# Performance work log

Hardware: AMD Instinct MI355X
Metric: run time of the kernel (lower is better)

## Reference

```python
import jax, jax.numpy as jnp
import numpy as np

B, DIM, H, W = 4, 64, 256, 256
HEADS = 8
HID = int(DIM * 2.66)  # 170, IEL hidden_features
EPS_LN = 1e-6


def setup_inputs() -> dict:
    key = jax.random.key(0)
    ks = jax.random.split(key, 16)
    r = lambda k, shape, s=0.02: jax.random.normal(k, shape, jnp.float32) * s
    return {
        "x": jax.random.normal(ks[0], (B, DIM, H, W), jnp.float32),
        "y": jax.random.normal(ks[1], (B, DIM, H, W), jnp.float32),
        # shared channels-first LayerNorm params
        "ln_w": jnp.ones((DIM,), jnp.float32),
        "ln_b": jnp.zeros((DIM,), jnp.float32),
        # CAB params (bias=False)
        "temperature": jnp.ones((HEADS, 1, 1), jnp.float32),
        "wq": r(ks[2], (DIM, DIM)),           # 1x1 conv: [out, in]
        "wq_dw": r(ks[3], (DIM, 1, 3, 3)),    # depthwise 3x3
        "wkv": r(ks[4], (2 * DIM, DIM)),
        "wkv_dw": r(ks[5], (2 * DIM, 1, 3, 3)),
        "w_proj": r(ks[6], (DIM, DIM)),
        # IEL params (bias=False)
        "w_in": r(ks[7], (2 * HID, DIM)),
        "w_dw": r(ks[8], (2 * HID, 1, 3, 3)),
        "w_dw1": r(ks[9], (HID, 1, 3, 3)),
        "w_dw2": r(ks[10], (HID, 1, 3, 3)),
        "w_out": r(ks[11], (DIM, HID)),
    }


def conv1x1(x, w):
    # x: [b,c,h,w], w: [o,c]
    return jnp.einsum('oc,bchw->bohw', w, x)


def dwconv3(x, w):
    # depthwise 3x3, SAME padding; w: [C,1,3,3]
    return jax.lax.conv_general_dilated(
        x, w, window_strides=(1, 1), padding='SAME',
        feature_group_count=x.shape[1],
        dimension_numbers=('NCHW', 'OIHW', 'NCHW'))


def layernorm_cf(x, w, b):
    # channels-first LayerNorm: mean/biased-var over channel dim
    u = jnp.mean(x, axis=1, keepdims=True)
    s = jnp.mean((x - u) ** 2, axis=1, keepdims=True)
    xn = (x - u) / jnp.sqrt(s + EPS_LN)
    return w[None, :, None, None] * xn + b[None, :, None, None]


def l2norm(x):
    # torch F.normalize(dim=-1): x / max(||x||, 1e-12)
    n = jnp.sqrt(jnp.sum(x * x, axis=-1, keepdims=True))
    return x / jnp.maximum(n, 1e-12)


def cab(x, y, temperature, wq, wq_dw, wkv, wkv_dw, w_proj):
    b, c, h, w = x.shape
    q = dwconv3(conv1x1(x, wq), wq_dw)
    kv = dwconv3(conv1x1(y, wkv), wkv_dw)
    k, v = kv[:, :c], kv[:, c:]
    ch = c // HEADS  # channels per head
    q = l2norm(q.reshape(b, HEADS, ch, h * w))
    k = l2norm(k.reshape(b, HEADS, ch, h * w))
    v = v.reshape(b, HEADS, ch, h * w)
    attn = jnp.einsum('bhce,bhde->bhcd', q, k) * temperature[None]  # [b,H,ch,ch]
    attn = jax.nn.softmax(attn, axis=-1)
    out = jnp.einsum('bhcd,bhde->bhce', attn, v).reshape(b, c, h, w)
    return conv1x1(out, w_proj)


def iel(x, w_in, w_dw, w_dw1, w_dw2, w_out):
    x = conv1x1(x, w_in)
    d = dwconv3(x, w_dw)
    x1, x2 = d[:, :HID], d[:, HID:]
    x1 = jnp.tanh(dwconv3(x1, w_dw1)) + x1
    x2 = jnp.tanh(dwconv3(x2, w_dw2)) + x2
    return conv1x1(x1 * x2, w_out)


def reference(x, y, ln_w, ln_b, temperature, wq, wq_dw, wkv, wkv_dw, w_proj,
              w_in, w_dw, w_dw1, w_dw2, w_out):
    # I_LCA block forward
    x = x + cab(layernorm_cf(x, ln_w, ln_b), layernorm_cf(y, ln_w, ln_b),
                temperature, wq, wq_dw, wkv, wkv_dw, w_proj)
    x = x + iel(layernorm_cf(x, ln_w, ln_b), w_in, w_dw, w_dw1, w_dw2, w_out)
    return x
```

## Files before the change

kernel.cpp:

```cpp
#include <hip/hip_runtime.h>
#include <hip/hip_bf16.h>

typedef __hip_bfloat16 bf16;
typedef unsigned short u16;
typedef unsigned int u32;
typedef __attribute__((ext_vector_type(8))) unsigned short ushort8;
typedef __attribute__((ext_vector_type(4))) unsigned int uint4_t;
typedef __attribute__((ext_vector_type(8))) short bf16x8;
typedef __attribute__((ext_vector_type(4))) short bf16x4;
typedef __attribute__((ext_vector_type(4))) float f32x4;
typedef __attribute__((ext_vector_type(2))) _Float16 half2_t;

#define PL 65536
#define EPS_LN 1e-6f

#if __has_builtin(__builtin_amdgcn_fdot2)
#define USE_FDOT2 1
#else
#define USE_FDOT2 0
#endif

__device__ __forceinline__ float fast_tanh(float v){
  float e = __expf(2.f*v);
  return 1.f - 2.f/(e+1.f);
}
__device__ __forceinline__ u16 f2bf(float f){
  bf16 h = __float2bfloat16(f);
  return __builtin_bit_cast(u16, h);
}
__device__ __forceinline__ float bf2f(u16 v){
  u32 u = ((u32)v) << 16;
  return __builtin_bit_cast(float, u);
}
__device__ __forceinline__ u16 f2h(float f){
  _Float16 h = (_Float16)f;
  return __builtin_bit_cast(u16, h);
}
__device__ __forceinline__ float h2f(u16 v){
  _Float16 h = __builtin_bit_cast(_Float16, v);
  return (float)h;
}
__device__ __forceinline__ float dot2h(u32 wpair, u32 kpair, float acc){
#if USE_FDOT2
  return __builtin_amdgcn_fdot2(__builtin_bit_cast(half2_t, wpair),
                                __builtin_bit_cast(half2_t, kpair), acc, false);
#else
  float a0 = h2f((u16)(wpair & 0xffff)), a1 = h2f((u16)(wpair >> 16));
  float k0 = h2f((u16)(kpair & 0xffff)), k1 = h2f((u16)(kpair >> 16));
  return acc + a0*k0 + a1*k1;
#endif
}
__device__ __forceinline__ u32 alignhalf(u32 hi, u32 lo){
  return (lo >> 16) | (hi << 16);
}

__global__ void convert_w(const float* __restrict__ wq, const float* __restrict__ wkv,
                          const float* __restrict__ win, const float* __restrict__ wout,
                          const float* __restrict__ wproj,
                          u16* __restrict__ Wq, u16* __restrict__ Wkv,
                          u16* __restrict__ Wp0, u16* __restrict__ Wp1,
                          u16* __restrict__ Wproj, u16* __restrict__ Wh){
  int stride = gridDim.x * 256;
  int gid = blockIdx.x * 256 + threadIdx.x;
  for (int i = gid; i < 64*64;  i += stride) Wq[i]  = f2bf(wq[i]);
  for (int i = gid; i < 128*64; i += stride) Wkv[i] = f2bf(wkv[i]);
  for (int i = gid; i < 176*64; i += stride) {
    int r = i >> 6, c = i & 63;
    Wp0[i] = (r < 85) ? f2bf(win[r*64+c]) : ((r < 170) ? f2bf(win[(85+r)*64+c]) : 0);
    Wp1[i] = (r < 85) ? f2bf(win[(85+r)*64+c]) : ((r < 170) ? f2bf(win[(170+r)*64+c]) : 0);
  }
  for (int i = gid; i < 64*64; i += stride) Wproj[i] = f2bf(wproj[i]);
  for (int i = gid; i < 64*192; i += stride) {
    int o = i / 192, c = i % 192;
    Wh[i] = (c < 170) ? f2bf(wout[o*170 + c]) : 0;
  }
}

__global__ __launch_bounds__(256) void ln_gemm(
    const float* __restrict__ x, const float* __restrict__ lnw,
    const float* __restrict__ lnb, const u16* __restrict__ W,
    u16* __restrict__ out, int MT, int Mvalid, int fmt) {
  int b  = blockIdx.y;
  int p0 = blockIdx.x * 256;
  int tid = threadIdx.x;
  int lane = tid & 63, wv = tid >> 6;
  __shared__ u16 shX[256][72];
  {
    const float* xb = x + ((size_t)b * 64) * PL + p0 + tid;
    float xn[64];
    float mu = 0.f;
    #pragma unroll
    for (int c = 0; c < 64; ++c) { xn[c] = xb[(size_t)c * PL]; mu += xn[c]; }
    mu *= (1.f/64.f);
    float var = 0.f;
    #pragma unroll
    for (int c = 0; c < 64; ++c) { float d = xn[c]-mu; var += d*d; }
    var *= (1.f/64.f);
    float inv = rsqrtf(var + EPS_LN);
    #pragma unroll
    for (int c8 = 0; c8 < 8; ++c8) {
      ushort8 pk;
      #pragma unroll
      for (int j = 0; j < 8; ++j)
        pk[j] = f2bf((xn[c8*8+j]-mu)*inv*lnw[c8*8+j] + lnb[c8*8+j]);
      *reinterpret_cast<ushort8*>(&shX[tid][c8*8]) = pk;
    }
  }
  __syncthreads();
  int col = lane & 15, kg = lane >> 4;
  int n0 = wv * 64;
  bf16x8 bfr[4][2];
  #pragma unroll
  for (int nt = 0; nt < 4; ++nt)
    #pragma unroll
    for (int kh = 0; kh < 2; ++kh)
      bfr[nt][kh] = *reinterpret_cast<const bf16x8*>(&shX[n0 + nt*16 + col][kh*32 + kg*8]);
  for (int mt = 0; mt < MT; ++mt) {
    bf16x8 a0 = *reinterpret_cast<const bf16x8*>(&W[(mt*16+col)*64      + kg*8]);
    bf16x8 a1 = *reinterpret_cast<const bf16x8*>(&W[(mt*16+col)*64 + 32 + kg*8]);
    #pragma unroll
    for (int nt = 0; nt < 4; ++nt) {
      f32x4 acc = {0.f,0.f,0.f,0.f};
      acc = __builtin_amdgcn_mfma_f32_16x16x32_bf16(a0, bfr[nt][0], acc, 0,0,0);
      acc = __builtin_amdgcn_mfma_f32_16x16x32_bf16(a1, bfr[nt][1], acc, 0,0,0);
      int mbase = mt*16 + kg*4;
      #pragma unroll
      for (int r = 0; r < 4; ++r) {
        int ch = mbase + r;
        if (ch < Mvalid)
          out[((size_t)b*Mvalid + ch)*PL + p0 + n0 + nt*16 + col] =
              fmt ? f2h(acc[r]) : f2bf(acc[r]);
      }
    }
  }
}

__global__ __launch_bounds__(256) void dwconv3v(
    const u16* __restrict__ in, const float* __restrict__ w9,
    u16* __restrict__ out, int C) {
  int plane = blockIdx.y;
  int cch = plane % C;
  int y0 = blockIdx.x * 8;
  int tid = threadIdx.x;
  const u16* ip = in + (size_t)plane * PL;
  __shared__ u16 sh[10][272];
  #pragma unroll
  for (int i = 0; i < 2; ++i) {
    int idx = tid + i*256;
    if (idx < 320) {
      int r = idx >> 5, seg = idx & 31;
      int gy = y0 - 1 + r;
      ushort8 v = {0,0,0,0,0,0,0,0};
      if (gy >= 0 && gy < 256)
        v = *reinterpret_cast<const ushort8*>(ip + gy*256 + seg*8);
      *reinterpret_cast<ushort8*>(&sh[r][8 + seg*8]) = v;
    }
  }
  if (tid < 10) { sh[tid][7] = 0; sh[tid][264] = 0; }
  __syncthreads();
  float wk[9];
  #pragma unroll
  for (int i=0;i<9;++i) wk[i] = w9[cch*9+i];
  int lr = tid >> 5, xs = (tid & 31) * 8;
  float row[3][10];
  #pragma unroll
  for (int i = 0; i < 3; ++i) {
    ushort8 m = *reinterpret_cast<const ushort8*>(&sh[lr+i][8+xs]);
    row[i][0] = bf2f(sh[lr+i][7+xs]);
    #pragma unroll
    for (int j=0;j<8;++j) row[i][1+j] = bf2f((u16)m[j]);
    row[i][9] = bf2f(sh[lr+i][16+xs]);
  }
  ushort8 o;
  #pragma unroll
  for (int j = 0; j < 8; ++j) {
    float a = 0.f;
    #pragma unroll
    for (int i=0;i<3;++i)
      #pragma unroll
      for (int k=0;k<3;++k) a += wk[i*3+k]*row[i][j+k];
    o[j] = f2bf(a);
  }
  int gy = y0 + lr;
  *reinterpret_cast<ushort8*>(out + (size_t)plane*PL + gy*256 + xs) = o;
}

__global__ __launch_bounds__(256) void attn_reduce1(
    const bf16* __restrict__ q, const bf16* __restrict__ kv,
    float* __restrict__ part) {
  int bh = blockIdx.y;
  int b = bh >> 3, h = bh & 7;
  int s = blockIdx.x;
  int t = threadIdx.x;
  int p = s*2048 + t*8;
  const u16* qb = reinterpret_cast<const u16*>(q)  + ((size_t)b*64  + h*8) * PL + p;
  const u16* kb = reinterpret_cast<const u16*>(kv) + ((size_t)b*128 + h*8) * PL + p;
  ushort8 vq[8], vk[8];
  #pragma unroll
  for (int c=0;c<8;++c) {
    vq[c] = *reinterpret_cast<const ushort8*>(qb + (size_t)c*PL);
    vk[c] = *reinterpret_cast<const ushort8*>(kb + (size_t)c*PL);
  }
  float acc[80];
  #pragma unroll
  for (int i=0;i<80;++i) acc[i]=0.f;
  #pragma unroll
  for (int e = 0; e < 8; ++e) {
    float qe[8], ke[8];
    #pragma unroll
    for (int c=0;c<8;++c) { qe[c]=bf2f((u16)vq[c][e]); ke[c]=bf2f((u16)vk[c][e]); }
    #pragma unroll
    for (int c=0;c<8;++c)
      #pragma unroll
      for (int d=0;d<8;++d) acc[c*8+d] += qe[c]*ke[d];
    #pragma unroll
    for (int c=0;c<8;++c) { acc[64+c] += qe[c]*qe[c]; acc[72+c] += ke[c]*ke[c]; }
  }
  __shared__ float lds[4][80];
  int lane = t & 63, wv = t >> 6;
  #pragma unroll
  for (int i=0;i<80;++i) {
    float v = acc[i];
    for (int off=32; off; off>>=1) v += __shfl_down(v, off);
    if (lane==0) lds[wv][i]=v;
  }
  __syncthreads();
  if (t < 80)
    part[((size_t)bh*32 + s)*80 + t] = lds[0][t]+lds[1][t]+lds[2][t]+lds[3][t];
}

__global__ void attn_reduce2(const float* __restrict__ part, float* __restrict__ red) {
  int bh = blockIdx.x; int t = threadIdx.x;
  if (t < 80) {
    float v = 0.f;
    for (int s=0;s<32;++s) v += part[((size_t)bh*32+s)*80+t];
    red[bh*80+t]=v;
  }
}

__global__ void attn_softmax(const float* __restrict__ red, const float* __restrict__ temp,
                             float* __restrict__ attn) {
  int bh = threadIdx.x;
  if (bh >= 32) return;
  int h = bh & 7;
  const float* r = red + bh*80;
  float nq[8], nk[8];
  for (int c=0;c<8;++c) nq[c] = fmaxf(sqrtf(r[64+c]), 1e-12f);
  for (int d=0;d<8;++d) nk[d] = fmaxf(sqrtf(r[72+d]), 1e-12f);
  float tm = temp[h];
  for (int c=0;c<8;++c) {
    float a[8]; float m=-1e30f;
    for (int d=0;d<8;++d){ a[d] = r[c*8+d]/(nq[c]*nk[d]) * tm; m=fmaxf(m,a[d]); }
    float ss=0.f;
    for (int d=0;d<8;++d){ a[d]=__expf(a[d]-m); ss+=a[d]; }
    float inv=1.f/ss;
    for (int d=0;d<8;++d) attn[bh*64 + c*8 + d] = a[d]*inv;
  }
}

__global__ __launch_bounds__(256) void attn_pv_proj(
    const bf16* __restrict__ kv, const float* __restrict__ attnb,
    const u16* __restrict__ Wp, const float* __restrict__ x,
    float* __restrict__ out) {
  int b  = blockIdx.y;
  int p0 = blockIdx.x * 256;
  int tid = threadIdx.x;
  int lane = tid & 63, wv = tid >> 6;
  __shared__ float at[512];
  __shared__ u16 shX[256][72];
  for (int i=tid; i<512; i+=256) at[i]=attnb[b*512+i];
  __syncthreads();
  {
    int pix = p0 + tid;
    const bf16* vb = kv + ((size_t)b*128 + 64)*PL + pix;
    #pragma unroll
    for (int h=0;h<8;++h){
      float vv[8];
      #pragma unroll
      for (int d=0;d<8;++d) vv[d]=__bfloat162float(vb[(size_t)(h*8+d)*PL]);
      ushort8 pk;
      #pragma unroll
      for (int c=0;c<8;++c){
        float acc=0.f;
        #pragma unroll
        for (int d=0;d<8;++d) acc += at[h*64+c*8+d]*vv[d];
        pk[c] = f2bf(acc);
      }
      *reinterpret_cast<ushort8*>(&shX[tid][h*8]) = pk;
    }
  }
  __syncthreads();
  int col = lane & 15, kg = lane >> 4;
  int n0 = wv * 64;
  bf16x8 bfr[4][2];
  #pragma unroll
  for (int nt = 0; nt < 4; ++nt)
    #pragma unroll
    for (int kh = 0; kh < 2; ++kh)
      bfr[nt][kh] = *reinterpret_cast<const bf16x8*>(&shX[n0 + nt*16 + col][kh*32 + kg*8]);
  #pragma unroll
  for (int mt = 0; mt < 4; ++mt) {
    bf16x8 a0 = *reinterpret_cast<const bf16x8*>(&Wp[(mt*16+col)*64      + kg*8]);
    bf16x8 a1 = *reinterpret_cast<const bf16x8*>(&Wp[(mt*16+col)*64 + 32 + kg*8]);
    #pragma unroll
    for (int nt = 0; nt < 4; ++nt) {
      f32x4 acc = {0.f,0.f,0.f,0.f};
      acc = __builtin_amdgcn_mfma_f32_16x16x32_bf16(a0, bfr[nt][0], acc, 0,0,0);
      acc = __builtin_amdgcn_mfma_f32_16x16x32_bf16(a1, bfr[nt][1], acc, 0,0,0);
      #pragma unroll
      for (int r = 0; r < 4; ++r) {
        int o = mt*16 + kg*4 + r;
        size_t idx = ((size_t)(b*64 + o))*PL + p0 + n0 + nt*16 + col;
        out[idx] = x[idx] + acc[r];
      }
    }
  }
}

__global__ __launch_bounds__(256) void iel_gate2(
    const u16* __restrict__ t, const float* __restrict__ wdw,
    const float* __restrict__ wdw1, const float* __restrict__ wdw2,
    u16* __restrict__ P, int hcbase) {
  int pj = blockIdx.y;
  int b = pj / 85, j = pj % 85;
  int hc = hcbase + j;
  int bx = blockIdx.x;
  int y0 = (bx >> 2) * 32;
  int x0 = (bx & 3) * 64;
  int tid = threadIdx.x;

  __shared__ u16 sT[2][36][80];
  __shared__ u16 sD[2][34][72];

  const u16* t1 = t + (size_t)(b*170 + j) * PL;
  const u16* t2 = t + (size_t)(b*170 + 85 + j) * PL;

  #pragma unroll
  for (int it = 0; it < 3; ++it) {
    int idx = tid + it*256;
    if (idx < 720) {
      int pl = idx / 360, rem = idx % 360;
      int r = rem / 10, ch = rem % 10;
      int gy = y0 + r - 2;
      int gxb = x0 - 8 + ch*8;
      ushort8 v = {0,0,0,0,0,0,0,0};
      if (gy >= 0 && gy < 256 && gxb >= 0 && gxb <= 248)
        v = *reinterpret_cast<const ushort8*>((pl ? t2 : t1) + gy*256 + gxb);
      *reinterpret_cast<ushort8*>(&sT[pl][r][ch*8]) = v;
    }
  }
  __syncthreads();

  #pragma unroll
  for (int it = 0; it < 3; ++it) {
    int idx = tid + it*256;
    if (idx < 612) {
      int pl = idx / 306, rem = idx % 306;
      int r = rem / 9, si = rem % 9;
      int gy = y0 + r - 1;
      const float* kp = wdw + (pl ? (170+hc) : hc)*9;
      u32 k01[3], k2z[3];
      #pragma unroll
      for (int i=0;i<3;++i){
        k01[i] = (u32)f2h(kp[i*3+0]) | ((u32)f2h(kp[i*3+1]) << 16);
        k2z[i] = (u32)f2h(kp[i*3+2]);
      }
      float a[8];
      #pragma unroll
      for (int jj=0;jj<8;++jj) a[jj]=0.f;
      #pragma unroll
      for (int i = 0; i < 3; ++i) {
        ushort8 A0 = *reinterpret_cast<const ushort8*>(&sT[pl][r+i][si*8]);
        ushort8 A1 = *reinterpret_cast<const ushort8*>(&sT[pl][r+i][si*8+8]);
        uint4_t wa = __builtin_bit_cast(uint4_t, A0);
        uint4_t wb = __builtin_bit_cast(uint4_t, A1);
        u32 R1=wa.y, R2=wa.z, R3=wa.w, R4=wb.x, R5=wb.y, R6=wb.z;
        u32 prs[10] = { alignhalf(R2,R1), R2, alignhalf(R3,R2), R3,
                        alignhalf(R4,R3), R4, alignhalf(R5,R4), R5,
                        alignhalf(R6,R5), R6 };
        #pragma unroll
        for (int jj = 0; jj < 8; ++jj)
          a[jj] = dot2h(prs[jj+2], k2z[i], dot2h(prs[jj], k01[i], a[jj]));
      }
      int gx0 = x0 + si*8 - 4;
      bool rowok = (gy >= 0 && gy < 256);
      ushort8 dv;
      #pragma unroll
      for (int jj = 0; jj < 8; ++jj) {
        int gx = gx0 + jj;
        bool ok = rowok && gx >= 0 && gx < 256;
        dv[jj] = ok ? f2h(a[jj]) : (u16)0;
      }
      *reinterpret_cast<ushort8*>(&sD[pl][r][si*8]) = dv;
    }
  }
  __syncthreads();

  int ry = tid >> 3, seg = tid & 7;
  float x1[8], x2[8];
  #pragma unroll
  for (int pl = 0; pl < 2; ++pl) {
    const float* kp = (pl ? wdw2 : wdw1) + hc*9;
    u32 k01[3], k2z[3];
    #pragma unroll
    for (int i=0;i<3;++i){
      k01[i] = (u32)f2h(kp[i*3+0]) | ((u32)f2h(kp[i*3+1]) << 16);
      k2z[i] = (u32)f2h(kp[i*3+2]);
    }
    float a[8];
    #pragma unroll
    for (int jj=0;jj<8;++jj) a[jj]=0.f;
    float dc[8];
    #pragma unroll
    for (int i = 0; i < 3; ++i) {
      ushort8 A0 = *reinterpret_cast<const ushort8*>(&sD[pl][ry+i][seg*8]);
      ushort8 A1 = *reinterpret_cast<const ushort8*>(&sD[pl][ry+i][seg*8+8]);
      uint4_t wa = __builtin_bit_cast(uint4_t, A0);
      uint4_t wb = __builtin_bit_cast(uint4_t, A1);
      u32 R1=wa.y, R2=wa.z, R3=wa.w, R4=wb.x, R5=wb.y, R6=wb.z;
      u32 prs[10] = { alignhalf(R2,R1), R2, alignhalf(R3,R2), R3,
                      alignhalf(R4,R3), R4, alignhalf(R5,R4), R5,
                      alignhalf(R6,R5), R6 };
      #pragma unroll
      for (int jj = 0; jj < 8; ++jj)
        a[jj] = dot2h(prs[jj+2], k2z[i], dot2h(prs[jj], k01[i], a[jj]));
      if (i == 1) {
        u32 cw[4] = { wa.z, wa.w, wb.x, wb.y };
        #pragma unroll
        for (int jj = 0; jj < 8; ++jj) {
          u32 wrd = cw[(jj+4)/2 - 2];
          u16 hv = (jj & 1) ? (u16)(wrd >> 16) : (u16)(wrd & 0xffff);
          dc[jj] = h2f(hv);
        }
      }
    }
    #pragma unroll
    for (int jj = 0; jj < 8; ++jj) {
      float g = fast_tanh(a[jj]) + dc[jj];
      if (pl) x2[jj] = g; else x1[jj] = g;
    }
  }
  ushort8 o;
  #pragma unroll
  for (int jj = 0; jj < 8; ++jj) o[jj] = f2bf(x1[jj]*x2[jj]);
  int gy = y0 + ry;
  *reinterpret_cast<ushort8*>(
      P + ((size_t)(b*170 + hcbase + j))*PL + gy*256 + x0 + seg*8) = o;
}

__global__ __launch_bounds__(256) void iel_gemm(
    const u16* __restrict__ Wh, const u16* __restrict__ P,
    float* __restrict__ out) {
  int b  = blockIdx.y;
  int p0 = blockIdx.x * 256;
  int tid = threadIdx.x;
  int lane = tid & 63, wv = tid >> 6;
  int col = lane & 15, kg = lane >> 4;
  int n0 = wv * 64;
  __shared__ u16 shP[256][36];
  f32x4 acc[4][4];
  #pragma unroll
  for (int mt=0;mt<4;++mt)
    #pragma unroll
    for (int nt=0;nt<4;++nt) acc[mt][nt] = (f32x4){0.f,0.f,0.f,0.f};

  int kk = tid & 31, q = tid >> 5;
  for (int c = 0; c < 6; ++c) {
    int hcl = c*32 + kk;
    ushort8 v[4];
    if (hcl < 170) {
      const u16* src = P + (size_t)(b*170 + hcl)*PL + p0 + q*32;
      #pragma unroll
      for (int jj=0;jj<4;++jj) v[jj] = *reinterpret_cast<const ushort8*>(src + jj*8);
    } else {
      #pragma unroll
      for (int jj=0;jj<4;++jj) v[jj] = (ushort8){0,0,0,0,0,0,0,0};
    }
    __syncthreads();
    #pragma unroll
    for (int jj=0;jj<4;++jj)
      #pragma unroll
      for (int i=0;i<8;++i) shP[q*32 + jj*8 + i][kk] = v[jj][i];
    __syncthreads();
    #pragma unroll
    for (int nt = 0; nt < 4; ++nt) {
      int px = n0 + nt*16 + col;
      const bf16x4* pp = reinterpret_cast<const bf16x4*>(&shP[px][kg*8]);
      bf16x4 plo = pp[0], phi = pp[1];
      bf16x8 bfrag;
      #pragma unroll
      for (int jj=0;jj<4;++jj){ bfrag[jj]=plo[jj]; bfrag[4+jj]=phi[jj]; }
      #pragma unroll
      for (int mt = 0; mt < 4; ++mt) {
        bf16x8 a = *reinterpret_cast<const bf16x8*>(&Wh[(mt*16+col)*192 + c*32 + kg*8]);
        acc[mt][nt] = __builtin_amdgcn_mfma_f32_16x16x32_bf16(a, bfrag, acc[mt][nt], 0,0,0);
      }
    }
  }
  #pragma unroll
  for (int mt=0; mt<4; ++mt)
    #pragma unroll
    for (int nt=0; nt<4; ++nt)
      #pragma unroll
      for (int r=0; r<4; ++r){
        int o = mt*16 + kg*4 + r;
        size_t idx = ((size_t)(b*64 + o))*PL + p0 + n0 + nt*16 + col;
        out[idx] += acc[mt][nt][r];
      }
}

extern "C" void kernel_launch(void* const* d_in, const int* in_sizes, int n_in,
                              void* d_out, int out_size, void* d_ws, size_t ws_size,
                              hipStream_t stream) {
  const float* x      = (const float*)d_in[0];
  const float* y      = (const float*)d_in[1];
  const float* lnw    = (const float*)d_in[2];
  const float* lnb    = (const float*)d_in[3];
  const float* temp   = (const float*)d_in[4];
  const float* wq     = (const float*)d_in[5];
  const float* wq_dw  = (const float*)d_in[6];
  const float* wkv    = (const float*)d_in[7];
  const float* wkv_dw = (const float*)d_in[8];
  const float* wproj  = (const float*)d_in[9];
  const float* w_in   = (const float*)d_in[10];
  const float* w_dw   = (const float*)d_in[11];
  const float* w_dw1  = (const float*)d_in[12];
  const float* w_dw2  = (const float*)d_in[13];
  const float* w_out  = (const float*)d_in[14];

  char* base = (char*)d_ws;
  u16* Wq_b    = (u16*)(base + 0);
  u16* Wkv_b   = (u16*)(base + 8192);
  u16* Wp0     = (u16*)(base + 24576);
  u16* Wp1     = (u16*)(base + 47104);
  u16* Wproj_b = (u16*)(base + 69632);
  u16* Wh      = (u16*)(base + 77824);
  char* A = base + 131072;

  u16*  kvpre = (u16*)A;
  u16*  kvd   = (u16*)(A + 89128960);
  u16*  qpre  = (u16*)A;
  u16*  qd    = (u16*)(A + 33554432);
  float* part = (float*)A;
  float* red  = (float*)(A + 1048576);
  float* attnb= (float*)(A + 1572864);
  u16*  tbuf  = (u16*)A;
  u16*  Pbuf  = (u16*)(A + 89128960);
  float* xmid = (float*)d_out;

  convert_w<<<64, 256, 0, stream>>>(wq, wkv, w_in, w_out, wproj,
                                    Wq_b, Wkv_b, Wp0, Wp1, Wproj_b, Wh);

  ln_gemm<<<dim3(256,4), 256, 0, stream>>>(y, lnw, lnb, Wkv_b, kvpre, 8, 128, 0);
  dwconv3v<<<dim3(32,512), 256, 0, stream>>>(kvpre, wkv_dw, kvd, 128);
  ln_gemm<<<dim3(256,4), 256, 0, stream>>>(x, lnw, lnb, Wq_b, qpre, 4, 64, 0);
  dwconv3v<<<dim3(32,256), 256, 0, stream>>>(qpre, wq_dw, qd, 64);
  attn_reduce1<<<dim3(32,32), 256, 0, stream>>>((const bf16*)qd, (const bf16*)kvd, part);
  attn_reduce2<<<32, 128, 0, stream>>>(part, red);
  attn_softmax<<<1, 64, 0, stream>>>(red, temp, attnb);
  attn_pv_proj<<<dim3(256,4), 256, 0, stream>>>((const bf16*)kvd, attnb, Wproj_b, x, xmid);

  ln_gemm<<<dim3(256,4), 256, 0, stream>>>(xmid, lnw, lnb, Wp0, tbuf, 11, 170, 1);
  iel_gate2<<<dim3(32,340), 256, 0, stream>>>(tbuf, w_dw, w_dw1, w_dw2, Pbuf, 0);
  ln_gemm<<<dim3(256,4), 256, 0, stream>>>(xmid, lnw, lnb, Wp1, tbuf, 11, 170, 1);
  iel_gate2<<<dim3(32,340), 256, 0, stream>>>(tbuf, w_dw, w_dw1, w_dw2, Pbuf, 85);
  iel_gemm<<<dim3(256,4), 256, 0, stream>>>(Wh, Pbuf, xmid);
}
```

Measured before the change: 462.9 us.

## Fuse second LayerNorm into proj epilogue, merge softmax kernels, reorder plane layout

The attention projection epilogue now also computes the residual-stream LayerNorm and writes a pixel-major bf16 normalized tensor. A new gemm_pm kernel consumes that tensor for both IEL input GEMMs, so xmid is no longer re-read and re-normalized twice. The attention reduce and softmax kernels are merged into one launch. kv and P planes are stored channel-major across the batch, and iel_gate2 remaps block indices to change scheduling order. This adds an extra pixel-major write and changes access strides. The xnb buffer shares its offset with Pbuf and is read after Pbuf is partly written, which may be an aliasing hazard.

```diff
diff --git a/kernel.cpp b/kernel.cpp
--- a/kernel.cpp
+++ b/kernel.cpp
@@ -5,6 +5,7 @@
 typedef unsigned short u16;
 typedef unsigned int u32;
 typedef __attribute__((ext_vector_type(8))) unsigned short ushort8;
+typedef __attribute__((ext_vector_type(4))) unsigned short us4;
 typedef __attribute__((ext_vector_type(4))) unsigned int uint4_t;
 typedef __attribute__((ext_vector_type(8))) short bf16x8;
 typedef __attribute__((ext_vector_type(4))) short bf16x4;
@@ -79,7 +80,7 @@
 __global__ __launch_bounds__(256) void ln_gemm(
     const float* __restrict__ x, const float* __restrict__ lnw,
     const float* __restrict__ lnb, const u16* __restrict__ W,
-    u16* __restrict__ out, int MT, int Mvalid, int fmt) {
+    u16* __restrict__ out, int MT, int Mvalid) {
   int b  = blockIdx.y;
   int p0 = blockIdx.x * 256;
   int tid = threadIdx.x;
@@ -128,8 +129,48 @@
       for (int r = 0; r < 4; ++r) {
         int ch = mbase + r;
         if (ch < Mvalid)
-          out[((size_t)b*Mvalid + ch)*PL + p0 + n0 + nt*16 + col] =
-              fmt ? f2h(acc[r]) : f2bf(acc[r]);
+          out[((size_t)b*Mvalid + ch)*PL + p0 + n0 + nt*16 + col] = f2bf(acc[r]);
+      }
+    }
+  }
+}
+
+__global__ __launch_bounds__(256) void gemm_pm(
+    const u16* __restrict__ xn, const u16* __restrict__ W,
+    u16* __restrict__ out, int MT, int Mvalid) {
+  int b  = blockIdx.y;
+  int p0 = blockIdx.x * 256;
+  int tid = threadIdx.x;
+  int lane = tid & 63, wv = tid >> 6;
+  __shared__ u16 shX[256][72];
+  const u16* src = xn + ((size_t)b * PL + p0) * 64;
+  #pragma unroll
+  for (int c8 = 0; c8 < 8; ++c8)
+    *reinterpret_cast<ushort8*>(&shX[tid][c8*8]) =
+        *reinterpret_cast<const ushort8*>(src + (size_t)tid*64 + c8*8);
+  __syncthreads();
+  int col = lane & 15, kg = lane >> 4;
+  int n0 = wv * 64;
+  bf16x8 bfr[4][2];
+  #pragma unroll
+  for (int nt = 0; nt < 4; ++nt)
+    #pragma unroll
+    for (int kh = 0; kh < 2; ++kh)
+      bfr[nt][kh] = *reinterpret_cast<const bf16x8*>(&shX[n0 + nt*16 + col][kh*32 + kg*8]);
+  for (int mt = 0; mt < MT; ++mt) {
+    bf16x8 a0 = *reinterpret_cast<const bf16x8*>(&W[(mt*16+col)*64      + kg*8]);
+    bf16x8 a1 = *reinterpret_cast<const bf16x8*>(&W[(mt*16+col)*64 + 32 + kg*8]);
+    #pragma unroll
+    for (int nt = 0; nt < 4; ++nt) {
+      f32x4 acc = {0.f,0.f,0.f,0.f};
+      acc = __builtin_amdgcn_mfma_f32_16x16x32_bf16(a0, bfr[nt][0], acc, 0,0,0);
+      acc = __builtin_amdgcn_mfma_f32_16x16x32_bf16(a1, bfr[nt][1], acc, 0,0,0);
+      int mbase = mt*16 + kg*4;
+      #pragma unroll
+      for (int r = 0; r < 4; ++r) {
+        int ch = mbase + r;
+        if (ch < Mvalid)
+          out[((size_t)b*Mvalid + ch)*PL + p0 + n0 + nt*16 + col] = f2h(acc[r]);
       }
     }
   }
@@ -137,9 +178,10 @@
 
 __global__ __launch_bounds__(256) void dwconv3v(
     const u16* __restrict__ in, const float* __restrict__ w9,
-    u16* __restrict__ out, int C) {
+    u16* __restrict__ out, int C, int cb) {
   int plane = blockIdx.y;
   int cch = plane % C;
+  int bb  = plane / C;
   int y0 = blockIdx.x * 8;
   int tid = threadIdx.x;
   const u16* ip = in + (size_t)plane * PL;
@@ -182,24 +224,25 @@
     o[j] = f2bf(a);
   }
   int gy = y0 + lr;
-  *reinterpret_cast<ushort8*>(out + (size_t)plane*PL + gy*256 + xs) = o;
+  int oplane = cb ? (cch*4 + bb) : plane;
+  *reinterpret_cast<ushort8*>(out + (size_t)oplane*PL + gy*256 + xs) = o;
 }
 
 __global__ __launch_bounds__(256) void attn_reduce1(
-    const bf16* __restrict__ q, const bf16* __restrict__ kv,
+    const u16* __restrict__ q, const u16* __restrict__ kv,
     float* __restrict__ part) {
   int bh = blockIdx.y;
   int b = bh >> 3, h = bh & 7;
   int s = blockIdx.x;
   int t = threadIdx.x;
   int p = s*2048 + t*8;
-  const u16* qb = reinterpret_cast<const u16*>(q)  + ((size_t)b*64  + h*8) * PL + p;
-  const u16* kb = reinterpret_cast<const u16*>(kv) + ((size_t)b*128 + h*8) * PL + p;
+  const u16* qb = q  + ((size_t)b*64 + h*8) * PL + p;
+  const u16* kb = kv + ((size_t)(h*8)*4 + b) * PL + p;
   ushort8 vq[8], vk[8];
   #pragma unroll
   for (int c=0;c<8;++c) {
     vq[c] = *reinterpret_cast<const ushort8*>(qb + (size_t)c*PL);
-    vk[c] = *reinterpret_cast<const ushort8*>(kb + (size_t)c*PL);
+    vk[c] = *reinterpret_cast<const ushort8*>(kb + (size_t)c*4*PL);
   }
   float acc[80];
   #pragma unroll
@@ -229,55 +272,58 @@
     part[((size_t)bh*32 + s)*80 + t] = lds[0][t]+lds[1][t]+lds[2][t]+lds[3][t];
 }
 
-__global__ void attn_reduce2(const float* __restrict__ part, float* __restrict__ red) {
+__global__ void attn_finish(const float* __restrict__ part, const float* __restrict__ temp,
+                            float* __restrict__ attn) {
   int bh = blockIdx.x; int t = threadIdx.x;
+  __shared__ float red[80];
   if (t < 80) {
     float v = 0.f;
     for (int s=0;s<32;++s) v += part[((size_t)bh*32+s)*80+t];
-    red[bh*80+t]=v;
-  }
-}
-
-__global__ void attn_softmax(const float* __restrict__ red, const float* __restrict__ temp,
-                             float* __restrict__ attn) {
-  int bh = threadIdx.x;
-  if (bh >= 32) return;
-  int h = bh & 7;
-  const float* r = red + bh*80;
-  float nq[8], nk[8];
-  for (int c=0;c<8;++c) nq[c] = fmaxf(sqrtf(r[64+c]), 1e-12f);
-  for (int d=0;d<8;++d) nk[d] = fmaxf(sqrtf(r[72+d]), 1e-12f);
-  float tm = temp[h];
-  for (int c=0;c<8;++c) {
+    red[t]=v;
+  }
+  __syncthreads();
+  if (t < 8) {
+    int c = t, h = bh & 7;
+    float nq = fmaxf(sqrtf(red[64+c]), 1e-12f);
+    float tm = temp[h];
     float a[8]; float m=-1e30f;
-    for (int d=0;d<8;++d){ a[d] = r[c*8+d]/(nq[c]*nk[d]) * tm; m=fmaxf(m,a[d]); }
+    #pragma unroll
+    for (int d=0;d<8;++d){
+      float nk = fmaxf(sqrtf(red[72+d]), 1e-12f);
+      a[d] = red[c*8+d]/(nq*nk) * tm; m=fmaxf(m,a[d]);
+    }
     float ss=0.f;
+    #pragma unroll
     for (int d=0;d<8;++d){ a[d]=__expf(a[d]-m); ss+=a[d]; }
     float inv=1.f/ss;
+    #pragma unroll
     for (int d=0;d<8;++d) attn[bh*64 + c*8 + d] = a[d]*inv;
   }
 }
 
 __global__ __launch_bounds__(256) void attn_pv_proj(
-    const bf16* __restrict__ kv, const float* __restrict__ attnb,
+    const u16* __restrict__ kv, const float* __restrict__ attnb,
     const u16* __restrict__ Wp, const float* __restrict__ x,
-    float* __restrict__ out) {
+    const float* __restrict__ lnw, const float* __restrict__ lnb,
+    float* __restrict__ out, u16* __restrict__ xnb) {
   int b  = blockIdx.y;
   int p0 = blockIdx.x * 256;
   int tid = threadIdx.x;
   int lane = tid & 63, wv = tid >> 6;
   __shared__ float at[512];
+  __shared__ float sw[64], sb[64];
   __shared__ u16 shX[256][72];
   for (int i=tid; i<512; i+=256) at[i]=attnb[b*512+i];
+  if (tid < 64) { sw[tid]=lnw[tid]; sb[tid]=lnb[tid]; }
   __syncthreads();
   {
     int pix = p0 + tid;
-    const bf16* vb = kv + ((size_t)b*128 + 64)*PL + pix;
+    const u16* vb = kv + ((size_t)(64*4) + b)*PL + pix;
     #pragma unroll
     for (int h=0;h<8;++h){
       float vv[8];
       #pragma unroll
-      for (int d=0;d<8;++d) vv[d]=__bfloat162float(vb[(size_t)(h*8+d)*PL]);
+      for (int d=0;d<8;++d) vv[d]=bf2f(vb[(size_t)((h*8+d)*4)*PL]);
       ushort8 pk;
       #pragma unroll
       for (int c=0;c<8;++c){
@@ -298,21 +344,54 @@
     #pragma unroll
     for (int kh = 0; kh < 2; ++kh)
       bfr[nt][kh] = *reinterpret_cast<const bf16x8*>(&shX[n0 + nt*16 + col][kh*32 + kg*8]);
+  f32x4 acc[4][4];
   #pragma unroll
   for (int mt = 0; mt < 4; ++mt) {
     bf16x8 a0 = *reinterpret_cast<const bf16x8*>(&Wp[(mt*16+col)*64      + kg*8]);
     bf16x8 a1 = *reinterpret_cast<const bf16x8*>(&Wp[(mt*16+col)*64 + 32 + kg*8]);
     #pragma unroll
     for (int nt = 0; nt < 4; ++nt) {
-      f32x4 acc = {0.f,0.f,0.f,0.f};
-      acc = __builtin_amdgcn_mfma_f32_16x16x32_bf16(a0, bfr[nt][0], acc, 0,0,0);
-      acc = __builtin_amdgcn_mfma_f32_16x16x32_bf16(a1, bfr[nt][1], acc, 0,0,0);
+      f32x4 a = {0.f,0.f,0.f,0.f};
+      a = __builtin_amdgcn_mfma_f32_16x16x32_bf16(a0, bfr[nt][0], a, 0,0,0);
+      a = __builtin_amdgcn_mfma_f32_16x16x32_bf16(a1, bfr[nt][1], a, 0,0,0);
+      acc[mt][nt] = a;
+    }
+  }
+  float s1[4] = {0.f,0.f,0.f,0.f}, s2[4] = {0.f,0.f,0.f,0.f};
+  #pragma unroll
+  for (int mt = 0; mt < 4; ++mt)
+    #pragma unroll
+    for (int nt = 0; nt < 4; ++nt)
       #pragma unroll
       for (int r = 0; r < 4; ++r) {
         int o = mt*16 + kg*4 + r;
         size_t idx = ((size_t)(b*64 + o))*PL + p0 + n0 + nt*16 + col;
-        out[idx] = x[idx] + acc[r];
-      }
+        float v = x[idx] + acc[mt][nt][r];
+        out[idx] = v;
+        acc[mt][nt][r] = v;
+        s1[nt] += v; s2[nt] += v*v;
+      }
+  #pragma unroll
+  for (int nt = 0; nt < 4; ++nt) {
+    s1[nt] += __shfl_xor(s1[nt], 16); s1[nt] += __shfl_xor(s1[nt], 32);
+    s2[nt] += __shfl_xor(s2[nt], 16); s2[nt] += __shfl_xor(s2[nt], 32);
+  }
+  #pragma unroll
+  for (int nt = 0; nt < 4; ++nt) {
+    float mu = s1[nt] * (1.f/64.f);
+    float var = s2[nt] * (1.f/64.f) - mu*mu;
+    float inv = rsqrtf(var + EPS_LN);
+    int pix = p0 + n0 + nt*16 + col;
+    u16* xp = xnb + ((size_t)b*PL + pix)*64 + kg*4;
+    #pragma unroll
+    for (int mt = 0; mt < 4; ++mt) {
+      us4 pk4;
+      #pragma unroll
+      for (int r = 0; r < 4; ++r) {
+        int ch = mt*16 + kg*4 + r;
+        pk4[r] = f2bf((acc[mt][nt][r]-mu)*inv*sw[ch] + sb[ch]);
+      }
+      *reinterpret_cast<us4*>(xp + mt*16) = pk4;
     }
   }
 }
@@ -321,10 +400,12 @@
     const u16* __restrict__ t, const float* __restrict__ wdw,
     const float* __restrict__ wdw1, const float* __restrict__ wdw2,
     u16* __restrict__ P, int hcbase) {
-  int pj = blockIdx.y;
+  int orig = blockIdx.x + (int)(gridDim.x * blockIdx.y);
+  int nb = (orig & 7) * 1360 + (orig >> 3);
+  int pj = nb >> 5;
+  int bx = nb & 31;
   int b = pj / 85, j = pj % 85;
   int hc = hcbase + j;
-  int bx = blockIdx.x;
   int y0 = (bx >> 2) * 32;
   int x0 = (bx & 3) * 64;
   int tid = threadIdx.x;
@@ -445,7 +526,7 @@
   for (int jj = 0; jj < 8; ++jj) o[jj] = f2bf(x1[jj]*x2[jj]);
   int gy = y0 + ry;
   *reinterpret_cast<ushort8*>(
-      P + ((size_t)(b*170 + hcbase + j))*PL + gy*256 + x0 + seg*8) = o;
+      P + ((size_t)((hcbase + j)*4 + b))*PL + gy*256 + x0 + seg*8) = o;
 }
 
 __global__ __launch_bounds__(256) void iel_gemm(
@@ -469,7 +550,7 @@
     int hcl = c*32 + kk;
     ushort8 v[4];
     if (hcl < 170) {
-      const u16* src = P + (size_t)(b*170 + hcl)*PL + p0 + q*32;
+      const u16* src = P + ((size_t)hcl*4 + b)*PL + p0 + q*32;
       #pragma unroll
       for (int jj=0;jj<4;++jj) v[jj] = *reinterpret_cast<const ushort8*>(src + jj*8);
     } else {
@@ -542,8 +623,8 @@
   u16*  qpre  = (u16*)A;
   u16*  qd    = (u16*)(A + 33554432);
   float* part = (float*)A;
-  float* red  = (float*)(A + 1048576);
   float* attnb= (float*)(A + 1572864);
+  u16*  xnb   = (u16*)(A + 89128960);
   u16*  tbuf  = (u16*)A;
   u16*  Pbuf  = (u16*)(A + 89128960);
   float* xmid = (float*)d_out;
@@ -551,18 +632,18 @@
   convert_w<<<64, 256, 0, stream>>>(wq, wkv, w_in, w_out, wproj,
                                     Wq_b, Wkv_b, Wp0, Wp1, Wproj_b, Wh);
 
-  ln_gemm<<<dim3(256,4), 256, 0, stream>>>(y, lnw, lnb, Wkv_b, kvpre, 8, 128, 0);
-  dwconv3v<<<dim3(32,512), 256, 0, stream>>>(kvpre, wkv_dw, kvd, 128);
-  ln_gemm<<<dim3(256,4), 256, 0, stream>>>(x, lnw, lnb, Wq_b, qpre, 4, 64, 0);
-  dwconv3v<<<dim3(32,256), 256, 0, stream>>>(qpre, wq_dw, qd, 64);
-  attn_reduce1<<<dim3(32,32), 256, 0, stream>>>((const bf16*)qd, (const bf16*)kvd, part);
-  attn_reduce2<<<32, 128, 0, stream>>>(part, red);
-  attn_softmax<<<1, 64, 0, stream>>>(red, temp, attnb);
-  attn_pv_proj<<<dim3(256,4), 256, 0, stream>>>((const bf16*)kvd, attnb, Wproj_b, x, xmid);
-
-  ln_gemm<<<dim3(256,4), 256, 0, stream>>>(xmid, lnw, lnb, Wp0, tbuf, 11, 170, 1);
+  ln_gemm<<<dim3(256,4), 256, 0, stream>>>(y, lnw, lnb, Wkv_b, kvpre, 8, 128);
+  dwconv3v<<<dim3(32,512), 256, 0, stream>>>(kvpre, wkv_dw, kvd, 128, 1);
+  ln_gemm<<<dim3(256,4), 256, 0, stream>>>(x, lnw, lnb, Wq_b, qpre, 4, 64);
+  dwconv3v<<<dim3(32,256), 256, 0, stream>>>(qpre, wq_dw, qd, 64, 0);
+  attn_reduce1<<<dim3(32,32), 256, 0, stream>>>(qd, kvd, part);
+  attn_finish<<<32, 128, 0, stream>>>(part, temp, attnb);
+  attn_pv_proj<<<dim3(256,4), 256, 0, stream>>>(kvd, attnb, Wproj_b, x, lnw, lnb,
+                                                xmid, xnb);
+
+  gemm_pm<<<dim3(256,4), 256, 0, stream>>>(xnb, Wp1, tbuf, 11, 170);
+  iel_gate2<<<dim3(32,340), 256, 0, stream>>>(tbuf, w_dw, w_dw1, w_dw2, Pbuf, 85);
+  gemm_pm<<<dim3(256,4), 256, 0, stream>>>(xnb, Wp0, tbuf, 11, 170);
   iel_gate2<<<dim3(32,340), 256, 0, stream>>>(tbuf, w_dw, w_dw1, w_dw2, Pbuf, 0);
-  ln_gemm<<<dim3(256,4), 256, 0, stream>>>(xmid, lnw, lnb, Wp1, tbuf, 11, 170, 1);
-  iel_gate2<<<dim3(32,340), 256, 0, stream>>>(tbuf, w_dw, w_dw1, w_dw2, Pbuf, 85);
   iel_gemm<<<dim3(256,4), 256, 0, stream>>>(Wh, Pbuf, xmid);
 }
```

After: 487.4 us. 1.05x slower.
